# Kernel optimization log

Hardware: AMD Instinct MI355X
Metric: run time of the kernel (lower is better)

## Reference

```python
import jax, jax.numpy as jnp
import numpy as np

DIM = 768
HEADS = 12
DIM_HEAD = 64
INNER = HEADS * DIM_HEAD
L = 256
EPS = 1e-08


def setup_inputs() -> dict:
    key = jax.random.key(0)
    k1, k2, k3, k4 = jax.random.split(key, 4)
    x = jax.random.normal(k1, (2, 4096, DIM), dtype=jnp.float32)
    # Linear weights stored torch-style: (out_features, in_features)
    w_qkv = jax.random.normal(k2, (3 * INNER, DIM), dtype=jnp.float32) * (DIM ** -0.5)
    w_out = jax.random.normal(k3, (DIM, INNER), dtype=jnp.float32) * (INNER ** -0.5)
    b_out = jax.random.normal(k4, (DIM,), dtype=jnp.float32) * 0.01
    # learned per-head log-scale temperature, init log2(L^2 - L)
    scale = jnp.full((HEADS,), np.log2(L * L - L), dtype=jnp.float32)
    return {"x": x, "w_qkv": w_qkv, "w_out": w_out, "b_out": b_out, "scale": scale}


def reference(x, w_qkv, w_out, b_out, scale):
    b, n, d = x.shape
    h, dh = HEADS, DIM_HEAD
    qkv = x @ w_qkv.T                                   # [b, n, 3*inner]
    q, k, v = jnp.split(qkv, 3, axis=-1)
    # [b, n, h, dh] -> [b, h, n, dh]
    q, k, v = (t.reshape(b, n, h, dh).transpose(0, 2, 1, 3) for t in (q, k, v))
    # Faithful to source: L2 norm over the HEADS axis (dim=1), then rsqrt
    q = q * jax.lax.rsqrt(jnp.linalg.norm(q, axis=1, keepdims=True) + EPS)
    k = k * jax.lax.rsqrt(jnp.linalg.norm(k, axis=1, keepdims=True) + EPS)
    dots = jnp.einsum('bhid,bhjd->bhij', q, k)          # [b, h, n, n]
    scores = jax.nn.softmax(dots / scale[:, None, None], axis=-1)
    out = jnp.einsum('bhij,bhjd->bhid', scores, v)      # [b, h, n, dh]
    out = out.transpose(0, 2, 1, 3).reshape(b, n, h * dh)
    return out @ w_out.T + b_out
```

## Files before the change

### kernel.cpp

```cpp
#include <hip/hip_runtime.h>
#include <hip/hip_bf16.h>

#define DIMX   768
#define HEADS  12
#define DH     64
#define INNER  768
#define NQKV   2304
#define SEQ    4096
#define BATCH  2
#define ROWS   (BATCH*SEQ)
#define EPSF   1e-8f
#define LOG2E  1.4426950408889634f

typedef __bf16 bf16x8 __attribute__((ext_vector_type(8)));
typedef float  f32x4  __attribute__((ext_vector_type(4)));
typedef float  f32x16 __attribute__((ext_vector_type(16)));

__device__ __forceinline__ unsigned short f2bf(float f) {
    unsigned int u = __float_as_uint(f);
    unsigned int r = ((u >> 16) & 1u) + 0x7FFFu;
    return (unsigned short)((u + r) >> 16);
}
__device__ __forceinline__ float bf2f(unsigned short u) {
    return __builtin_bit_cast(float, (unsigned)u << 16);
}
__device__ __forceinline__ unsigned pkbf(float a, float b) {
    unsigned short la = __builtin_bit_cast(unsigned short, (__bf16)a);
    unsigned short lb = __builtin_bit_cast(unsigned short, (__bf16)b);
    return (unsigned)la | ((unsigned)lb << 16);
}

__global__ __launch_bounds__(256) void cast_f32_bf16(
    const float* __restrict__ src, unsigned short* __restrict__ dst, int n)
{
    int i = (blockIdx.x * 256 + threadIdx.x) * 4;
    if (i + 3 < n) {
        float4 v = *reinterpret_cast<const float4*>(src + i);
        ushort4 o;
        o.x = f2bf(v.x); o.y = f2bf(v.y); o.z = f2bf(v.z); o.w = f2bf(v.w);
        *reinterpret_cast<ushort4*>(dst + i) = o;
    }
}

template<bool BF16OUT>
__global__ __launch_bounds__(256) void gemm_bt_kernel(
    const unsigned short* __restrict__ A,
    const unsigned short* __restrict__ B,
    void* __restrict__ Cv,
    const float* __restrict__ bias,
    int M, int N, int K)
{
    __shared__ unsigned short shA[128][72];
    __shared__ unsigned short shB[128][72];

    const int bm0 = blockIdx.x * 128;
    const int bn0 = blockIdx.y * 128;
    const int tid = threadIdx.x;
    const int lane = tid & 63;
    const int wid  = tid >> 6;
    const int l15  = lane & 15;
    const int l4   = lane >> 4;
    const int wr   = wid >> 1;
    const int wc   = wid & 1;

    f32x4 acc[4][4];
    #pragma unroll
    for (int i = 0; i < 4; ++i)
        #pragma unroll
        for (int j = 0; j < 4; ++j)
            acc[i][j] = (f32x4){0.f, 0.f, 0.f, 0.f};

    const int nkt = K >> 6;
    for (int kt = 0; kt < nkt; ++kt) {
        const int k0 = kt << 6;
        __syncthreads();
        #pragma unroll
        for (int it = 0; it < 4; ++it) {
            int c = tid + it * 256;
            int row = c >> 3, colc = c & 7;
            *reinterpret_cast<uint4*>(&shA[row][colc * 8]) =
                *reinterpret_cast<const uint4*>(&A[(size_t)(bm0 + row) * K + k0 + colc * 8]);
            *reinterpret_cast<uint4*>(&shB[row][colc * 8]) =
                *reinterpret_cast<const uint4*>(&B[(size_t)(bn0 + row) * K + k0 + colc * 8]);
        }
        __syncthreads();
        #pragma unroll
        for (int ks = 0; ks < 2; ++ks) {
            bf16x8 af[4], bfr[4];
            #pragma unroll
            for (int mf = 0; mf < 4; ++mf)
                af[mf] = *reinterpret_cast<const bf16x8*>(&shA[wr * 64 + mf * 16 + l15][ks * 32 + l4 * 8]);
            #pragma unroll
            for (int nf = 0; nf < 4; ++nf)
                bfr[nf] = *reinterpret_cast<const bf16x8*>(&shB[wc * 64 + nf * 16 + l15][ks * 32 + l4 * 8]);
            #pragma unroll
            for (int mf = 0; mf < 4; ++mf)
                #pragma unroll
                for (int nf = 0; nf < 4; ++nf)
                    acc[mf][nf] = __builtin_amdgcn_mfma_f32_16x16x32_bf16(
                        af[mf], bfr[nf], acc[mf][nf], 0, 0, 0);
        }
    }

    #pragma unroll
    for (int mf = 0; mf < 4; ++mf) {
        #pragma unroll
        for (int nf = 0; nf < 4; ++nf) {
            int col = bn0 + wc * 64 + nf * 16 + l15;
            float badd = bias ? bias[col] : 0.f;
            #pragma unroll
            for (int r = 0; r < 4; ++r) {
                int row = bm0 + wr * 64 + mf * 16 + l4 * 4 + r;
                if constexpr (BF16OUT)
                    ((unsigned short*)Cv)[(size_t)row * N + col] = f2bf(acc[mf][nf][r] + badd);
                else
                    ((float*)Cv)[(size_t)row * N + col] = acc[mf][nf][r] + badd;
            }
        }
    }
}

__global__ __launch_bounds__(256) void normalize_kernel(
    const unsigned short* __restrict__ qkv,
    const float* __restrict__ scale,
    unsigned short* __restrict__ qo,
    unsigned short* __restrict__ ko)
{
    int t = blockIdx.x * 256 + threadIdx.x;
    int row = t >> 6;
    int d = t & 63;
    int b = row >> 12;
    int n = row & 4095;
    const unsigned short* base = qkv + (size_t)row * NQKV;

    float qv[12], kv[12];
    float sq = 0.f, sk = 0.f;
    #pragma unroll
    for (int h = 0; h < 12; ++h) {
        qv[h] = bf2f(base[h * 64 + d]);
        kv[h] = bf2f(base[768 + h * 64 + d]);
        sq += qv[h] * qv[h];
        sk += kv[h] * kv[h];
    }
    float rq = rsqrtf(sqrtf(sq) + EPSF);
    float rk = rsqrtf(sqrtf(sk) + EPSF);
    #pragma unroll
    for (int h = 0; h < 12; ++h) {
        size_t bh = (size_t)(b * 12 + h);
        float fold = LOG2E / scale[h];
        qo[(bh * SEQ + n) * 64 + d] = f2bf(qv[h] * rq * fold);
        ko[(bh * SEQ + n) * 64 + d] = f2bf(kv[h] * rk);
    }
}

__global__ __launch_bounds__(256) void vtrans_kernel(
    const unsigned short* __restrict__ qkv,
    unsigned short* __restrict__ vt)
{
    __shared__ unsigned short tile[64][72];
    const int bh = blockIdx.x;
    const int nt = blockIdx.y;
    const int b = bh / HEADS, h = bh % HEADS;
    const int tid = threadIdx.x;

    #pragma unroll
    for (int it = 0; it < 2; ++it) {
        int c = tid + it * 256;
        int r = c >> 3, cc = c & 7;
        *reinterpret_cast<uint4*>(&tile[r][cc * 8]) =
            *reinterpret_cast<const uint4*>(
                &qkv[(size_t)(b * SEQ + nt * 64 + r) * NQKV + 1536 + h * 64 + cc * 8]);
    }
    __syncthreads();
    #pragma unroll
    for (int it = 0; it < 2; ++it) {
        int c = tid + it * 256;
        int d = c >> 3, nc = c & 7;
        ushort4 o0, o1;
        o0.x = tile[nc * 8 + 0][d]; o0.y = tile[nc * 8 + 1][d];
        o0.z = tile[nc * 8 + 2][d]; o0.w = tile[nc * 8 + 3][d];
        o1.x = tile[nc * 8 + 4][d]; o1.y = tile[nc * 8 + 5][d];
        o1.z = tile[nc * 8 + 6][d]; o1.w = tile[nc * 8 + 7][d];
        unsigned short* dst = &vt[((size_t)bh * 64 + d) * SEQ + nt * 64 + nc * 8];
        *reinterpret_cast<ushort4*>(dst)     = o0;
        *reinterpret_cast<ushort4*>(dst + 4) = o1;
    }
}

__global__ __launch_bounds__(256) void attn_kernel(
    const unsigned short* __restrict__ qg,
    const unsigned short* __restrict__ kg,
    const unsigned short* __restrict__ vtg,
    float* __restrict__ po,
    float* __restrict__ pl)
{
    __shared__ unsigned short shK[64][72];
    __shared__ unsigned short shV[64][72];

    const int qblk = blockIdx.x;
    const int bh   = blockIdx.y;
    const int g    = blockIdx.z;
    const int tid  = threadIdx.x;
    const int lane = tid & 63;
    const int wid  = tid >> 6;
    const int l31  = lane & 31;
    const int hi   = lane >> 5;

    bf16x8 qf[4];
    {
        const unsigned short* qrow =
            qg + ((size_t)bh * SEQ + qblk * 128 + wid * 32 + l31) * 64 + hi * 8;
        #pragma unroll
        for (int d0 = 0; d0 < 4; ++d0)
            qf[d0] = *reinterpret_cast<const bf16x8*>(qrow + d0 * 16);
    }

    f32x16 ot[2];
    #pragma unroll
    for (int r = 0; r < 16; ++r) { ot[0][r] = 0.f; ot[1][r] = 0.f; }
    float l_lane = 0.f;

    const unsigned short* kbase = kg  + ((size_t)bh * SEQ + g * 2048) * 64;
    const unsigned short* vbase = vtg + (size_t)bh * 64 * SEQ + g * 2048;

    for (int kt = 0; kt < 32; ++kt) {
        __syncthreads();
        #pragma unroll
        for (int it = 0; it < 2; ++it) {
            int c = tid + it * 256;
            int row = c >> 3, colc = c & 7;
            *reinterpret_cast<uint4*>(&shK[row][colc * 8]) =
                *reinterpret_cast<const uint4*>(&kbase[(size_t)(kt * 64 + row) * 64 + colc * 8]);
            *reinterpret_cast<uint4*>(&shV[row][colc * 8]) =
                *reinterpret_cast<const uint4*>(&vbase[(size_t)row * SEQ + kt * 64 + colc * 8]);
        }
        __syncthreads();

        f32x16 st0, st1;
        #pragma unroll
        for (int r = 0; r < 16; ++r) { st0[r] = 0.f; st1[r] = 0.f; }
        #pragma unroll
        for (int d0 = 0; d0 < 4; ++d0) {
            bf16x8 kf0 = *reinterpret_cast<const bf16x8*>(&shK[l31][d0 * 16 + hi * 8]);
            bf16x8 kf1 = *reinterpret_cast<const bf16x8*>(&shK[32 + l31][d0 * 16 + hi * 8]);
            st0 = __builtin_amdgcn_mfma_f32_32x32x16_bf16(kf0, qf[d0], st0, 0, 0, 0);
            st1 = __builtin_amdgcn_mfma_f32_32x32x16_bf16(kf1, qf[d0], st1, 0, 0, 0);
        }

        float s0 = 0.f, s1 = 0.f, s2 = 0.f, s3 = 0.f;
        unsigned cp0[8], cp1[8];
        #pragma unroll
        for (int t = 0; t < 8; ++t) {
            float pa = __builtin_amdgcn_exp2f(st0[2 * t]);
            float pb = __builtin_amdgcn_exp2f(st0[2 * t + 1]);
            float pc = __builtin_amdgcn_exp2f(st1[2 * t]);
            float pd = __builtin_amdgcn_exp2f(st1[2 * t + 1]);
            s0 += pa; s1 += pb; s2 += pc; s3 += pd;
            cp0[t] = pkbf(pa, pb);
            cp1[t] = pkbf(pc, pd);
        }
        l_lane += (s0 + s1) + (s2 + s3);

        #pragma unroll
        for (int cb = 0; cb < 2; ++cb) {
            #pragma unroll
            for (int kk = 0; kk < 2; ++kk) {
                unsigned c0 = cb ? cp1[4 * kk + 0] : cp0[4 * kk + 0];
                unsigned c1 = cb ? cp1[4 * kk + 1] : cp0[4 * kk + 1];
                unsigned c2 = cb ? cp1[4 * kk + 2] : cp0[4 * kk + 2];
                unsigned c3 = cb ? cp1[4 * kk + 3] : cp0[4 * kk + 3];
                unsigned e0 = __shfl_xor(c0, 32);
                unsigned e1 = __shfl_xor(c1, 32);
                unsigned e2 = __shfl_xor(c2, 32);
                unsigned e3 = __shfl_xor(c3, 32);
                union { unsigned uu[4]; bf16x8 v; } pu;
                pu.uu[0] = hi ? e2 : c0;
                pu.uu[1] = hi ? e3 : c1;
                pu.uu[2] = hi ? c2 : e0;
                pu.uu[3] = hi ? c3 : e1;
                #pragma unroll
                for (int df = 0; df < 2; ++df) {
                    bf16x8 vf = *reinterpret_cast<const bf16x8*>(
                        &shV[df * 32 + l31][cb * 32 + kk * 16 + hi * 8]);
                    ot[df] = __builtin_amdgcn_mfma_f32_32x32x16_bf16(vf, pu.v, ot[df], 0, 0, 0);
                }
            }
        }
    }

    float l_all = l_lane + __shfl_xor(l_lane, 32);
    int n = qblk * 128 + wid * 32 + l31;
    float* prow = po + ((size_t)(g * 24 + bh) * SEQ + n) * 64;
    #pragma unroll
    for (int df = 0; df < 2; ++df) {
        #pragma unroll
        for (int t = 0; t < 4; ++t) {
            float4 v = make_float4(ot[df][4 * t], ot[df][4 * t + 1],
                                   ot[df][4 * t + 2], ot[df][4 * t + 3]);
            *reinterpret_cast<float4*>(prow + df * 32 + t * 8 + hi * 4) = v;
        }
    }
    if (hi == 0)
        pl[(size_t)(g * 24 + bh) * SEQ + n] = l_all;
}

__global__ __launch_bounds__(256) void combine_kernel(
    const float* __restrict__ po,
    const float* __restrict__ pl,
    unsigned short* __restrict__ attnout)
{
    int idx = blockIdx.x * 256 + threadIdx.x;
    int oct = idx & 7;
    int q   = (idx >> 3) & 4095;
    int bh  = idx >> 15;
    int b = bh / HEADS, h = bh % HEADS;
    int d0 = oct * 8;

    size_t base = ((size_t)bh * SEQ + q) * 64 + d0;
    const float* p0 = po + base;
    const float* p1 = po + (size_t)24 * SEQ * 64 + base;
    float4 a0 = *reinterpret_cast<const float4*>(p0);
    float4 a1 = *reinterpret_cast<const float4*>(p0 + 4);
    float4 b0 = *reinterpret_cast<const float4*>(p1);
    float4 b1 = *reinterpret_cast<const float4*>(p1 + 4);
    float l = pl[(size_t)bh * SEQ + q] + pl[(size_t)24 * SEQ + bh * SEQ + q];
    float inv = 1.0f / l;

    unsigned w0 = pkbf((a0.x + b0.x) * inv, (a0.y + b0.y) * inv);
    unsigned w1 = pkbf((a0.z + b0.z) * inv, (a0.w + b0.w) * inv);
    unsigned w2 = pkbf((a1.x + b1.x) * inv, (a1.y + b1.y) * inv);
    unsigned w3 = pkbf((a1.z + b1.z) * inv, (a1.w + b1.w) * inv);
    uint4 ov = make_uint4(w0, w1, w2, w3);
    *reinterpret_cast<uint4*>(&attnout[((size_t)(b * SEQ + q)) * INNER + h * 64 + d0]) = ov;
}

extern "C" void kernel_launch(void* const* d_in, const int* in_sizes, int n_in,
                              void* d_out, int out_size, void* d_ws, size_t ws_size,
                              hipStream_t stream)
{
    const float* x      = (const float*)d_in[0];
    const float* w_qkv  = (const float*)d_in[1];
    const float* w_out  = (const float*)d_in[2];
    const float* b_out  = (const float*)d_in[3];
    const float* scale  = (const float*)d_in[4];
    float* out = (float*)d_out;
    char* ws = (char*)d_ws;

    unsigned short* xb    = (unsigned short*)(ws);
    unsigned short* wqkvb = (unsigned short*)(ws + 12582912);
    unsigned short* woutb = (unsigned short*)(ws + 16121856);
    unsigned short* attnb = (unsigned short*)(ws + 17301504);
    unsigned short* qb    = (unsigned short*)(ws + 29884416);
    unsigned short* kb    = (unsigned short*)(ws + 42467328);
    unsigned short* vtb   = (unsigned short*)(ws + 55050240);
    unsigned short* qkvb  = (unsigned short*)(ws + 67633152);
    float*          po    = (float*)(ws + 67633152);
    float*          pl    = (float*)(ws + 117964800);

    cast_f32_bf16<<<6144, 256, 0, stream>>>(x, xb, 6291456);
    cast_f32_bf16<<<1728, 256, 0, stream>>>(w_qkv, wqkvb, 1769472);
    cast_f32_bf16<<<576, 256, 0, stream>>>(w_out, woutb, 589824);

    gemm_bt_kernel<true><<<dim3(64, 18), 256, 0, stream>>>(xb, wqkvb, qkvb, nullptr, ROWS, NQKV, DIMX);

    normalize_kernel<<<2048, 256, 0, stream>>>(qkvb, scale, qb, kb);
    vtrans_kernel<<<dim3(BATCH * HEADS, SEQ / 64), 256, 0, stream>>>(qkvb, vtb);

    attn_kernel<<<dim3(SEQ / 128, BATCH * HEADS, 2), 256, 0, stream>>>(qb, kb, vtb, po, pl);
    combine_kernel<<<3072, 256, 0, stream>>>(po, pl, attnb);

    gemm_bt_kernel<false><<<dim3(64, 6), 256, 0, stream>>>(attnb, woutb, out, b_out, ROWS, INNER, INNER);
}
```

Before: 263.8 us.

## Use direct global-to-LDS loads, XCD-aware block mapping, and permlane32 swaps

The GEMM now stages A and B tiles with global_load_lds (direct global-to-LDS DMA) into unpadded 64-wide shared arrays. Its 2D grid becomes a 1D grid remapped so neighbouring M tiles land on the same XCD. The attention kernel gets a similar XCD-grouped mapping of (bh, qblk), and it processes the two 32-key halves sequentially to reduce register pressure. The shfl_xor plus select exchange of probabilities is replaced by permlane32_swap. Removing the LDS padding may bring bank conflicts on the MFMA fragment reads.

After: 280.9 us. 6.5% more time.

```diff
diff --git a/kernel.cpp b/kernel.cpp
--- a/kernel.cpp
+++ b/kernel.cpp
@@ -15,6 +15,7 @@
 typedef __bf16 bf16x8 __attribute__((ext_vector_type(8)));
 typedef float  f32x4  __attribute__((ext_vector_type(4)));
 typedef float  f32x16 __attribute__((ext_vector_type(16)));
+typedef unsigned u32x2 __attribute__((ext_vector_type(2)));
 
 __device__ __forceinline__ unsigned short f2bf(float f) {
     unsigned int u = __float_as_uint(f);
@@ -28,6 +29,12 @@
     unsigned short la = __builtin_bit_cast(unsigned short, (__bf16)a);
     unsigned short lb = __builtin_bit_cast(unsigned short, (__bf16)b);
     return (unsigned)la | ((unsigned)lb << 16);
+}
+
+__device__ __forceinline__ void gload_lds16(const void* g, void* l) {
+    __builtin_amdgcn_global_load_lds(
+        (const __attribute__((address_space(1))) void*)g,
+        (__attribute__((address_space(3))) void*)l, 16, 0, 0);
 }
 
 __global__ __launch_bounds__(256) void cast_f32_bf16(
@@ -48,13 +55,15 @@
     const unsigned short* __restrict__ B,
     void* __restrict__ Cv,
     const float* __restrict__ bias,
-    int M, int N, int K)
-{
-    __shared__ unsigned short shA[128][72];
-    __shared__ unsigned short shB[128][72];
-
-    const int bm0 = blockIdx.x * 128;
-    const int bn0 = blockIdx.y * 128;
+    int M, int N, int K, int bmx)
+{
+    __shared__ unsigned short shA[128][64];
+    __shared__ unsigned short shB[128][64];
+
+    const int xcd = blockIdx.x & 7;
+    const int idx = blockIdx.x >> 3;
+    const int bm0 = (xcd * bmx + (idx % bmx)) * 128;
+    const int bn0 = (idx / bmx) * 128;
     const int tid = threadIdx.x;
     const int lane = tid & 63;
     const int wid  = tid >> 6;
@@ -62,6 +71,8 @@
     const int l4   = lane >> 4;
     const int wr   = wid >> 1;
     const int wc   = wid & 1;
+    const int srow = lane >> 3;
+    const int scol = (lane & 7) * 8;
 
     f32x4 acc[4][4];
     #pragma unroll
@@ -75,13 +86,10 @@
         const int k0 = kt << 6;
         __syncthreads();
         #pragma unroll
-        for (int it = 0; it < 4; ++it) {
-            int c = tid + it * 256;
-            int row = c >> 3, colc = c & 7;
-            *reinterpret_cast<uint4*>(&shA[row][colc * 8]) =
-                *reinterpret_cast<const uint4*>(&A[(size_t)(bm0 + row) * K + k0 + colc * 8]);
-            *reinterpret_cast<uint4*>(&shB[row][colc * 8]) =
-                *reinterpret_cast<const uint4*>(&B[(size_t)(bn0 + row) * K + k0 + colc * 8]);
+        for (int j = 0; j < 4; ++j) {
+            int row = wid * 32 + j * 8;
+            gload_lds16(&A[(size_t)(bm0 + row + srow) * K + k0 + scol], &shA[row][0]);
+            gload_lds16(&B[(size_t)(bn0 + row + srow) * K + k0 + scol], &shB[row][0]);
         }
         __syncthreads();
         #pragma unroll
@@ -197,9 +205,13 @@
     __shared__ unsigned short shK[64][72];
     __shared__ unsigned short shV[64][72];
 
-    const int qblk = blockIdx.x;
-    const int bh   = blockIdx.y;
-    const int g    = blockIdx.z;
+    const int wg   = blockIdx.x;
+    const int xcd  = wg & 7;
+    const int slot = wg >> 3;
+    const int bh   = xcd * 3 + (slot >> 5);
+    const int qblk = slot & 31;
+    const int g    = blockIdx.y;
+
     const int tid  = threadIdx.x;
     const int lane = tid & 63;
     const int wid  = tid >> 6;
@@ -236,52 +248,44 @@
         }
         __syncthreads();
 
-        f32x16 st0, st1;
-        #pragma unroll
-        for (int r = 0; r < 16; ++r) { st0[r] = 0.f; st1[r] = 0.f; }
-        #pragma unroll
-        for (int d0 = 0; d0 < 4; ++d0) {
-            bf16x8 kf0 = *reinterpret_cast<const bf16x8*>(&shK[l31][d0 * 16 + hi * 8]);
-            bf16x8 kf1 = *reinterpret_cast<const bf16x8*>(&shK[32 + l31][d0 * 16 + hi * 8]);
-            st0 = __builtin_amdgcn_mfma_f32_32x32x16_bf16(kf0, qf[d0], st0, 0, 0, 0);
-            st1 = __builtin_amdgcn_mfma_f32_32x32x16_bf16(kf1, qf[d0], st1, 0, 0, 0);
-        }
-
-        float s0 = 0.f, s1 = 0.f, s2 = 0.f, s3 = 0.f;
-        unsigned cp0[8], cp1[8];
-        #pragma unroll
-        for (int t = 0; t < 8; ++t) {
-            float pa = __builtin_amdgcn_exp2f(st0[2 * t]);
-            float pb = __builtin_amdgcn_exp2f(st0[2 * t + 1]);
-            float pc = __builtin_amdgcn_exp2f(st1[2 * t]);
-            float pd = __builtin_amdgcn_exp2f(st1[2 * t + 1]);
-            s0 += pa; s1 += pb; s2 += pc; s3 += pd;
-            cp0[t] = pkbf(pa, pb);
-            cp1[t] = pkbf(pc, pd);
-        }
-        l_lane += (s0 + s1) + (s2 + s3);
-
-        #pragma unroll
-        for (int cb = 0; cb < 2; ++cb) {
+        #pragma unroll
+        for (int c = 0; c < 2; ++c) {
+            f32x16 st;
+            #pragma unroll
+            for (int r = 0; r < 16; ++r) st[r] = 0.f;
+            #pragma unroll
+            for (int d0 = 0; d0 < 4; ++d0) {
+                bf16x8 kf = *reinterpret_cast<const bf16x8*>(
+                    &shK[c * 32 + l31][d0 * 16 + hi * 8]);
+                st = __builtin_amdgcn_mfma_f32_32x32x16_bf16(kf, qf[d0], st, 0, 0, 0);
+            }
+
+            float s0 = 0.f, s1 = 0.f;
+            unsigned cp[8];
+            #pragma unroll
+            for (int t = 0; t < 8; ++t) {
+                float pa = __builtin_amdgcn_exp2f(st[2 * t]);
+                float pb = __builtin_amdgcn_exp2f(st[2 * t + 1]);
+                s0 += pa; s1 += pb;
+                cp[t] = pkbf(pa, pb);
+            }
+            l_lane += s0 + s1;
+
             #pragma unroll
             for (int kk = 0; kk < 2; ++kk) {
-                unsigned c0 = cb ? cp1[4 * kk + 0] : cp0[4 * kk + 0];
-                unsigned c1 = cb ? cp1[4 * kk + 1] : cp0[4 * kk + 1];
-                unsigned c2 = cb ? cp1[4 * kk + 2] : cp0[4 * kk + 2];
-                unsigned c3 = cb ? cp1[4 * kk + 3] : cp0[4 * kk + 3];
-                unsigned e0 = __shfl_xor(c0, 32);
-                unsigned e1 = __shfl_xor(c1, 32);
-                unsigned e2 = __shfl_xor(c2, 32);
-                unsigned e3 = __shfl_xor(c3, 32);
+                u32x2 s = __builtin_amdgcn_permlane32_swap(
+                    cp[4 * kk + 0], cp[4 * kk + 2], false, false);
+                u32x2 t = __builtin_amdgcn_permlane32_swap(
+                    cp[4 * kk + 1], cp[4 * kk + 3], false, false);
                 union { unsigned uu[4]; bf16x8 v; } pu;
-                pu.uu[0] = hi ? e2 : c0;
-                pu.uu[1] = hi ? e3 : c1;
-                pu.uu[2] = hi ? c2 : e0;
-                pu.uu[3] = hi ? c3 : e1;
+                pu.uu[0] = s.x;
+                pu.uu[1] = t.x;
+                pu.uu[2] = s.y;
+                pu.uu[3] = t.y;
                 #pragma unroll
                 for (int df = 0; df < 2; ++df) {
                     bf16x8 vf = *reinterpret_cast<const bf16x8*>(
-                        &shV[df * 32 + l31][cb * 32 + kk * 16 + hi * 8]);
+                        &shV[df * 32 + l31][c * 32 + kk * 16 + hi * 8]);
                     ot[df] = __builtin_amdgcn_mfma_f32_32x32x16_bf16(vf, pu.v, ot[df], 0, 0, 0);
                 }
             }
@@ -361,13 +365,13 @@
     cast_f32_bf16<<<1728, 256, 0, stream>>>(w_qkv, wqkvb, 1769472);
     cast_f32_bf16<<<576, 256, 0, stream>>>(w_out, woutb, 589824);
 
-    gemm_bt_kernel<true><<<dim3(64, 18), 256, 0, stream>>>(xb, wqkvb, qkvb, nullptr, ROWS, NQKV, DIMX);
+    gemm_bt_kernel<true><<<1152, 256, 0, stream>>>(xb, wqkvb, qkvb, nullptr, ROWS, NQKV, DIMX, 8);
 
     normalize_kernel<<<2048, 256, 0, stream>>>(qkvb, scale, qb, kb);
     vtrans_kernel<<<dim3(BATCH * HEADS, SEQ / 64), 256, 0, stream>>>(qkvb, vtb);
 
-    attn_kernel<<<dim3(SEQ / 128, BATCH * HEADS, 2), 256, 0, stream>>>(qb, kb, vtb, po, pl);
+    attn_kernel<<<dim3(768, 2), 256, 0, stream>>>(qb, kb, vtb, po, pl);
     combine_kernel<<<3072, 256, 0, stream>>>(po, pl, attnb);
 
-    gemm_bt_kernel<false><<<dim3(64, 6), 256, 0, stream>>>(attnb, woutb, out, b_out, ROWS, INNER, INNER);
-}
+    gemm_bt_kernel<false><<<384, 256, 0, stream>>>(attnb, woutb, out, b_out, ROWS, INNER, INNER, 8);
+}
```
